# Optimization experiments

Hardware: AMD Instinct MI355X
Metric: run time of the kernel (lower is better)

## Reference

```python
import jax, jax.numpy as jnp
import numpy as np

N, E = 50000, 800000          # nodes, edges
IN, H1, D1 = 128, 8, 32       # gcn1: 8 heads x 32 -> concat 256
HID1 = H1 * D1                # 256
HID2 = 128                    # gcn2: 1 head x 128
FC1, OUT = 512, 1
NEG_SLOPE = 0.2


def _nrm(k, shape, s=0.05):
    return jax.random.normal(k, shape, jnp.float32) * s


def setup_inputs() -> dict:
    key = jax.random.key(0)
    ks = jax.random.split(key, 16)
    return {
        "x": jax.random.normal(ks[0], (N, IN), jnp.float32),
        "edge_index": jax.random.randint(ks[1], (2, E), 0, N, dtype=jnp.int32),
        # gcn1 params
        "W1": _nrm(ks[2], (IN, H1 * D1)),
        "att_src1": _nrm(ks[3], (H1, D1)),
        "att_dst1": _nrm(ks[4], (H1, D1)),
        "b1": jnp.zeros((HID1,), jnp.float32),
        # gcn2 params (1 head)
        "W2": _nrm(ks[5], (HID1, HID2)),
        "att_src2": _nrm(ks[6], (1, HID2)),
        "att_dst2": _nrm(ks[7], (1, HID2)),
        "b2": jnp.zeros((HID2,), jnp.float32),
        # fc head
        "fcW1": _nrm(ks[8], (HID2, FC1)),
        "fcb1": jnp.zeros((FC1,), jnp.float32),
        "fcW2": _nrm(ks[9], (FC1, OUT)),
        "fcb2": jnp.zeros((OUT,), jnp.float32),
    }


def gat_layer(x, src, dst, W, a_src, a_dst, b, heads, dim):
    """PyG GATConv (eval mode): gather -> segment-softmax over dst -> scatter."""
    n = x.shape[0]
    h = (x @ W).reshape(n, heads, dim)                     # [N,H,D]
    a_s = jnp.einsum('nhd,hd->nh', h, a_src)               # [N,H]
    a_d = jnp.einsum('nhd,hd->nh', h, a_dst)
    e = jax.nn.leaky_relu(a_s[src] + a_d[dst], NEG_SLOPE)  # [E,H]
    m = jax.ops.segment_max(e, dst, num_segments=n)        # [N,H]
    m = jnp.where(jnp.isfinite(m), m, 0.0)                 # empty segments
    ex = jnp.exp(e - m[dst])
    denom = jax.ops.segment_sum(ex, dst, num_segments=n)
    alpha = ex / (denom[dst] + 1e-16)                      # [E,H]
    out = jax.ops.segment_sum(h[src] * alpha[:, :, None], dst, num_segments=n)
    return out.reshape(n, heads * dim) + b, alpha


def reference(x, edge_index, W1, att_src1, att_dst1, b1,
              W2, att_src2, att_dst2, b2, fcW1, fcb1, fcW2, fcb2):
    src, dst = edge_index[0], edge_index[1]
    x1, alpha1 = gat_layer(x, src, dst, W1, att_src1, att_dst1, b1, H1, D1)
    x1 = jax.nn.elu(x1)
    x2, alpha2 = gat_layer(x1, src, dst, W2, att_src2, att_dst2, b2, 1, HID2)
    x2 = jax.nn.relu(x2)
    h = jax.nn.relu(x2 @ fcW1 + fcb1)
    out = h @ fcW2 + fcb2                                  # [N,1]
    return out, alpha1, alpha2
```

## Files before the change

kernel.cpp:

```cpp
#include <hip/hip_runtime.h>
#include <hip/hip_bf16.h>
#include <hip/hip_fp8.h>
#include <math.h>

#define NN 50000
#define EE 800000
#define IN_DIM 128
#define H1 8
#define D1 32
#define HID1 256
#define HID2 128
#define FC1 512
#define NEG_SLOPE 0.2f
#define NREP 16

typedef short v8s __attribute__((ext_vector_type(8)));
typedef float v4f __attribute__((ext_vector_type(4)));
typedef float v2f __attribute__((ext_vector_type(2)));
typedef unsigned int v4u __attribute__((ext_vector_type(4)));

__device__ __forceinline__ float bf2f(unsigned short u) {
    unsigned int x = ((unsigned int)u) << 16;
    return __uint_as_float(x);
}
__device__ __forceinline__ unsigned short f2bf(float v) {
    __hip_bfloat16 h = __float2bfloat16(v);
    return *(unsigned short*)&h;
}
__device__ __forceinline__ unsigned char f2f8(float v) {
    __hip_fp8_e4m3 t(v);
    return (unsigned char)t.__x;
}
__device__ __forceinline__ float f8tof(unsigned char u) {
    __hip_fp8_e4m3 t;
    t.__x = (__hip_fp8_storage_t)u;
    return (float)t;
}

__device__ __forceinline__ void f8x4(unsigned int w, float& f0, float& f1, float& f2, float& f3) {
#if __has_builtin(__builtin_amdgcn_cvt_pk_f32_fp8)
    v2f lo = __builtin_amdgcn_cvt_pk_f32_fp8((int)w, false);
    v2f hi = __builtin_amdgcn_cvt_pk_f32_fp8((int)w, true);
    f0 = lo[0]; f1 = lo[1]; f2 = hi[0]; f3 = hi[1];
#else
    f0 = f8tof((unsigned char)(w & 0xff));
    f1 = f8tof((unsigned char)((w >> 8) & 0xff));
    f2 = f8tof((unsigned char)((w >> 16) & 0xff));
    f3 = f8tof((unsigned char)(w >> 24));
#endif
}


__global__ void hist_kernel(const int* __restrict__ dst, int* __restrict__ counts_rep) {
    int e = blockIdx.x * blockDim.x + threadIdx.x;
    if (e >= EE) return;
    int r = blockIdx.x & (NREP - 1);
    atomicAdd(&counts_rep[r * NN + dst[e]], 1);
}

__global__ void reduce_kernel(const int* __restrict__ counts_rep, int* __restrict__ counts_total) {
    int d = blockIdx.x * blockDim.x + threadIdx.x;
    if (d >= NN) return;
    int t = 0;
    #pragma unroll
    for (int r = 0; r < NREP; r++) t += counts_rep[r * NN + d];
    counts_total[d] = t;
}

__global__ __launch_bounds__(256) void scan_a_kernel(const int* __restrict__ counts,
                                                     int* __restrict__ excl,
                                                     int* __restrict__ bsum, int n) {
    __shared__ int wsum[4];
    int tid = threadIdx.x;
    int base = blockIdx.x * 1024 + tid * 4;
    int v0 = 0, v1 = 0, v2 = 0, v3 = 0;
    if (base + 3 < n) {
        int4 t = *(const int4*)(counts + base);
        v0 = t.x; v1 = t.y; v2 = t.z; v3 = t.w;
    } else {
        if (base + 0 < n) v0 = counts[base + 0];
        if (base + 1 < n) v1 = counts[base + 1];
        if (base + 2 < n) v2 = counts[base + 2];
        if (base + 3 < n) v3 = counts[base + 3];
    }
    int tot = v0 + v1 + v2 + v3;
    int lane = tid & 63;
    int w = tid >> 6;
    int x = tot;
    #pragma unroll
    for (int off = 1; off < 64; off <<= 1) {
        int y = __shfl_up(x, off);
        if (lane >= off) x += y;
    }
    if (lane == 63) wsum[w] = x;
    __syncthreads();
    int woff = 0;
    for (int i = 0; i < w; i++) woff += wsum[i];
    int et = woff + x - tot;
    if (base + 0 < n) excl[base + 0] = et;
    if (base + 1 < n) excl[base + 1] = et + v0;
    if (base + 2 < n) excl[base + 2] = et + v0 + v1;
    if (base + 3 < n) excl[base + 3] = et + v0 + v1 + v2;
    if (tid == 255) bsum[blockIdx.x] = woff + x;
}

__global__ __launch_bounds__(64) void scan_b_kernel(int* __restrict__ bsum,
                                                    int* __restrict__ row_ptr, int nb, int n) {
    int lane = threadIdx.x;
    int v = (lane < nb) ? bsum[lane] : 0;
    int x = v;
    #pragma unroll
    for (int off = 1; off < 64; off <<= 1) {
        int y = __shfl_up(x, off);
        if (lane >= off) x += y;
    }
    if (lane < nb) bsum[lane] = x - v;
    if (lane == 63) row_ptr[n] = x;
}

__global__ __launch_bounds__(256) void scan_c_kernel(const int* __restrict__ excl,
                                                     const int* __restrict__ bsum,
                                                     int* __restrict__ row_ptr, int n) {
    int base = blockIdx.x * 1024 + threadIdx.x * 4;
    int off = bsum[blockIdx.x];
    #pragma unroll
    for (int j = 0; j < 4; j++) {
        int i = base + j;
        if (i < n) row_ptr[i] = excl[i] + off;
    }
}

__global__ void base_kernel(const int* __restrict__ row_ptr, const int* __restrict__ counts_rep,
                            int* __restrict__ cursor_rep) {
    int d = blockIdx.x * blockDim.x + threadIdx.x;
    if (d >= NN) return;
    int running = row_ptr[d];
    #pragma unroll
    for (int r = 0; r < NREP; r++) {
        cursor_rep[r * NN + d] = running;
        running += counts_rep[r * NN + d];
    }
}

__global__ void scatter_kernel(const int* __restrict__ src, const int* __restrict__ dst,
                               int* __restrict__ cursor_rep, int2* __restrict__ pairs) {
    int e = blockIdx.x * blockDim.x + threadIdx.x;
    if (e >= EE) return;
    int r = blockIdx.x & (NREP - 1);
    int d = dst[e];
    int p = atomicAdd(&cursor_rep[r * NN + d], 1);
    pairs[p] = make_int2(e, src[e]);
}


__device__ __forceinline__ void pack_one(const float* __restrict__ B,
                                         __hip_bfloat16* __restrict__ Bp,
                                         int K, int N, int idx) {
    int k = idx / N, n = idx % N;
    int ntile = n >> 4, ks = k >> 5, kk = k & 31;
    int lane = (n & 15) | ((kk >> 3) << 4);
    int j = kk & 7;
    int KS = K >> 5;
    Bp[((size_t)(ntile * KS + ks) * 64 + lane) * 8 + j] = __float2bfloat16(B[idx]);
}

__global__ void prep_kernel(const float* __restrict__ x, __hip_bfloat16* __restrict__ xbf,
                            const float* __restrict__ W1, __hip_bfloat16* __restrict__ W1p,
                            const float* __restrict__ W2, __hip_bfloat16* __restrict__ W2p,
                            const float* __restrict__ fcW1, __hip_bfloat16* __restrict__ fW1p) {
    int i = blockIdx.x * blockDim.x + threadIdx.x;
    const int N0 = NN * IN_DIM;
    const int N1 = N0 + IN_DIM * HID1;
    const int N2 = N1 + HID1 * HID2;
    const int N3 = N2 + HID2 * FC1;
    if (i < N0) xbf[i] = __float2bfloat16(x[i]);
    else if (i < N1) pack_one(W1, W1p, IN_DIM, HID1, i - N0);
    else if (i < N2) pack_one(W2, W2p, HID1, HID2, i - N1);
    else if (i < N3) pack_one(fcW1, fW1p, HID2, FC1, i - N2);
}


template <int ATT>
__global__ __launch_bounds__(256) void mgemm_kernel(const __hip_bfloat16* __restrict__ A,
                                                    const __hip_bfloat16* __restrict__ Bp,
                                                    unsigned char* __restrict__ Cf8,
                                                    const float* __restrict__ as_w,
                                                    const float* __restrict__ ad_w,
                                                    float* __restrict__ a_s,
                                                    float* __restrict__ a_d,
                                                    int M, int K, int N) {
    int w = threadIdx.x >> 6, l = threadIdx.x & 63;
    int bm = blockIdx.x * 128 + w * 32;
    int bn = blockIdx.y * 64;
    int lr = l & 15, lk = l >> 4;
    int KS = K >> 5;
    const short* Ab = (const short*)A;
    const short* Bb = (const short*)Bp;
    v4f acc[2][4];
    #pragma unroll
    for (int mi = 0; mi < 2; mi++)
        #pragma unroll
        for (int nt = 0; nt < 4; nt++) acc[mi][nt] = (v4f)(0.f);
    for (int ks = 0; ks < KS; ks++) {
        v8s a[2];
        #pragma unroll
        for (int mi = 0; mi < 2; mi++) {
            int gm = bm + mi * 16 + lr;
            a[mi] = (gm < M) ? *(const v8s*)(Ab + (size_t)gm * K + ks * 32 + lk * 8)
                             : (v8s)(short)0;
        }
        #pragma unroll
        for (int nt = 0; nt < 4; nt++) {
            int ntile = (bn >> 4) + nt;
            v8s b = *(const v8s*)(Bb + ((size_t)(ntile * KS + ks) * 64 + l) * 8);
            acc[0][nt] = __builtin_amdgcn_mfma_f32_16x16x32_bf16(a[0], b, acc[0][nt], 0, 0, 0);
            acc[1][nt] = __builtin_amdgcn_mfma_f32_16x16x32_bf16(a[1], b, acc[1][nt], 0, 0, 0);
        }
    }
    #pragma unroll
    for (int mi = 0; mi < 2; mi++) {
        #pragma unroll
        for (int nt = 0; nt < 4; nt++) {
            int gn = bn + nt * 16 + lr;
            #pragma unroll
            for (int j = 0; j < 4; j++) {
                int gm = bm + mi * 16 + lk * 4 + j;
                if (gm < M)
                    Cf8[(size_t)gm * N + gn] = f2f8(acc[mi][nt][j]);
            }
        }
    }
    float ws0 = as_w[bn + lr], ws1 = as_w[bn + 16 + lr];
    float ws2 = as_w[bn + 32 + lr], ws3 = as_w[bn + 48 + lr];
    float wd0 = ad_w[bn + lr], wd1 = ad_w[bn + 16 + lr];
    float wd2 = ad_w[bn + 32 + lr], wd3 = ad_w[bn + 48 + lr];
    float sA[2][4], dA[2][4], sB[2][4], dB[2][4];
    #pragma unroll
    for (int mi = 0; mi < 2; mi++)
        #pragma unroll
        for (int j = 0; j < 4; j++) {
            if constexpr (ATT == 1) {
                sA[mi][j] = acc[mi][0][j] * ws0 + acc[mi][1][j] * ws1;
                sB[mi][j] = acc[mi][2][j] * ws2 + acc[mi][3][j] * ws3;
                dA[mi][j] = acc[mi][0][j] * wd0 + acc[mi][1][j] * wd1;
                dB[mi][j] = acc[mi][2][j] * wd2 + acc[mi][3][j] * wd3;
            } else {
                sA[mi][j] = acc[mi][0][j] * ws0 + acc[mi][1][j] * ws1
                          + acc[mi][2][j] * ws2 + acc[mi][3][j] * ws3;
                dA[mi][j] = acc[mi][0][j] * wd0 + acc[mi][1][j] * wd1
                          + acc[mi][2][j] * wd2 + acc[mi][3][j] * wd3;
                sB[mi][j] = 0.f; dB[mi][j] = 0.f;
            }
        }
    #pragma unroll
    for (int off = 1; off < 16; off <<= 1) {
        #pragma unroll
        for (int mi = 0; mi < 2; mi++)
            #pragma unroll
            for (int j = 0; j < 4; j++) {
                sA[mi][j] += __shfl_xor(sA[mi][j], off);
                dA[mi][j] += __shfl_xor(dA[mi][j], off);
                if constexpr (ATT == 1) {
                    sB[mi][j] += __shfl_xor(sB[mi][j], off);
                    dB[mi][j] += __shfl_xor(dB[mi][j], off);
                }
            }
    }
    if (lr == 0) {
        #pragma unroll
        for (int mi = 0; mi < 2; mi++)
            #pragma unroll
            for (int j = 0; j < 4; j++) {
                int row = bm + mi * 16 + lk * 4 + j;
                if (row < M) {
                    if constexpr (ATT == 1) {
                        int h0 = bn >> 5;
                        a_s[(size_t)row * 8 + h0]     = sA[mi][j];
                        a_s[(size_t)row * 8 + h0 + 1] = sB[mi][j];
                        a_d[(size_t)row * 8 + h0]     = dA[mi][j];
                        a_d[(size_t)row * 8 + h0 + 1] = dB[mi][j];
                    } else {
                        atomicAdd(&a_s[row], sA[mi][j]);
                        atomicAdd(&a_d[row], dA[mi][j]);
                    }
                }
            }
    }
}


__global__ __launch_bounds__(256) void fc_mfma_kernel(const __hip_bfloat16* __restrict__ A,
                                                      const __hip_bfloat16* __restrict__ Bp,
                                                      const float* __restrict__ fcb1,
                                                      const float* __restrict__ fcW2,
                                                      const float* __restrict__ fcb2,
                                                      float* __restrict__ out) {
    __shared__ float red[4][32];
    int w = threadIdx.x >> 6, l = threadIdx.x & 63;
    int bm = blockIdx.x * 32;
    int lr = l & 15, lk = l >> 4;
    const int K = HID2, KS = K >> 5;
    const short* Ab = (const short*)A;
    const short* Bb = (const short*)Bp;
    v4f acc[2][8];
    #pragma unroll
    for (int mi = 0; mi < 2; mi++)
        #pragma unroll
        for (int nt = 0; nt < 8; nt++) acc[mi][nt] = (v4f)(0.f);
    for (int ks = 0; ks < KS; ks++) {
        v8s a[2];
        #pragma unroll
        for (int mi = 0; mi < 2; mi++) {
            int gm = bm + mi * 16 + lr;
            a[mi] = (gm < NN) ? *(const v8s*)(Ab + (size_t)gm * K + ks * 32 + lk * 8)
                              : (v8s)(short)0;
        }
        #pragma unroll
        for (int nt = 0; nt < 8; nt++) {
            int ntile = w * 8 + nt;
            v8s b = *(const v8s*)(Bb + ((size_t)(ntile * KS + ks) * 64 + l) * 8);
            acc[0][nt] = __builtin_amdgcn_mfma_f32_16x16x32_bf16(a[0], b, acc[0][nt], 0, 0, 0);
            acc[1][nt] = __builtin_amdgcn_mfma_f32_16x16x32_bf16(a[1], b, acc[1][nt], 0, 0, 0);
        }
    }
    float p[2][4];
    #pragma unroll
    for (int mi = 0; mi < 2; mi++)
        #pragma unroll
        for (int j = 0; j < 4; j++) p[mi][j] = 0.f;
    #pragma unroll
    for (int nt = 0; nt < 8; nt++) {
        int col = w * 128 + nt * 16 + lr;
        float b1v = fcb1[col], w2v = fcW2[col];
        #pragma unroll
        for (int mi = 0; mi < 2; mi++) {
            #pragma unroll
            for (int j = 0; j < 4; j++) {
                float v = acc[mi][nt][j] + b1v;
                p[mi][j] += ((v > 0.f) ? v : 0.f) * w2v;
            }
        }
    }
    #pragma unroll
    for (int mi = 0; mi < 2; mi++)
        #pragma unroll
        for (int j = 0; j < 4; j++) {
            float v = p[mi][j];
            v += __shfl_xor(v, 1);
            v += __shfl_xor(v, 2);
            v += __shfl_xor(v, 4);
            v += __shfl_xor(v, 8);
            p[mi][j] = v;
        }
    if (lr == 0) {
        #pragma unroll
        for (int mi = 0; mi < 2; mi++)
            #pragma unroll
            for (int j = 0; j < 4; j++) red[w][mi * 16 + lk * 4 + j] = p[mi][j];
    }
    __syncthreads();
    int tid = threadIdx.x;
    if (tid < 32) {
        int gm = bm + tid;
        if (gm < NN)
            out[gm] = red[0][tid] + red[1][tid] + red[2][tid] + red[3][tid] + fcb2[0];
    }
}


template <int KM>
__device__ __forceinline__ void gat1_fast(int lane, int start, int cnt,
                                          const int2* __restrict__ pairs,
                                          const float* __restrict__ a_s, float ad,
                                          const unsigned char* __restrict__ hf8,
                                          float* __restrict__ alpha1_out,
                                          float& acc0, float& acc1, float& acc2, float& acc3) {
    int h = lane & 7, j = lane >> 3;
    int hl = lane >> 3;
    int cl = min(lane, cnt - 1);
    int2 ep = pairs[start + cl];
    int e_all = ep.x, s_all = ep.y;
    unsigned int loff = (unsigned int)(lane << 2);

    if constexpr (KM <= 4) {
        constexpr int NB = KM * 8;
        int sj[KM];
        float ev[KM];
        #pragma unroll
        for (int k = 0; k < KM; k++) {
            int idx = j + k * 8;
            sj[k] = __shfl(s_all, idx);
            ev[k] = a_s[(size_t)sj[k] * 8 + h];
        }
        unsigned int qt[NB];
        #pragma unroll
        for (int e = 0; e < NB; e++) {
            int sje = __shfl(s_all, e);
            qt[e] = *(const unsigned int*)(hf8 + (((unsigned int)sje << 8) | loff));
        }
        float ex[KM];
        #pragma unroll
        for (int k = 0; k < KM; k++) {
            int idx = j + k * 8;
            float v = ev[k] + ad;
            v = (v >= 0.f) ? v : NEG_SLOPE * v;
            ex[k] = (idx < cnt) ? v : -INFINITY;
        }
        float m = ex[0];
        #pragma unroll
        for (int k = 1; k < KM; k++) m = fmaxf(m, ex[k]);
        m = fmaxf(m, __shfl_xor(m, 8));
        m = fmaxf(m, __shfl_xor(m, 16));
        m = fmaxf(m, __shfl_xor(m, 32));
        float s = 0.f;
        #pragma unroll
        for (int k = 0; k < KM; k++) {
            ex[k] = expf(ex[k] - m);
            s += ex[k];
        }
        s += __shfl_xor(s, 8);
        s += __shfl_xor(s, 16);
        s += __shfl_xor(s, 32);
        float inv = 1.f / (s + 1e-16f);
        #pragma unroll
        for (int k = 0; k < KM; k++) ex[k] *= inv;
        #pragma unroll
        for (int k = 0; k < KM; k++) {
            int idx = j + k * 8;
            int eo = __shfl(e_all, idx);
            if (idx < cnt) alpha1_out[(size_t)eo * 8 + h] = ex[k];
        }
        #pragma unroll
        for (int e = 0; e < NB; e++) {
            float At = __shfl(ex[e >> 3], (e & 7) * 8 + hl);
            float f0, f1, f2, f3;
            f8x4(qt[e], f0, f1, f2, f3);
            acc0 += At * f0;
            acc1 += At * f1;
            acc2 += At * f2;
            acc3 += At * f3;
        }
    } else {
        float ex[KM];
        int sj[KM];
        #pragma unroll
        for (int k = 0; k < KM; k++) {
            int idx = j + k * 8;
            sj[k] = __shfl(s_all, idx);
            float v = a_s[(size_t)sj[k] * 8 + h] + ad;
            v = (v >= 0.f) ? v : NEG_SLOPE * v;
            ex[k] = (idx < cnt) ? v : -INFINITY;
        }
        float m = ex[0];
        #pragma unroll
        for (int k = 1; k < KM; k++) m = fmaxf(m, ex[k]);
        m = fmaxf(m, __shfl_xor(m, 8));
        m = fmaxf(m, __shfl_xor(m, 16));
        m = fmaxf(m, __shfl_xor(m, 32));
        float s = 0.f;
        #pragma unroll
        for (int k = 0; k < KM; k++) {
            ex[k] = expf(ex[k] - m);
            s += ex[k];
        }
        s += __shfl_xor(s, 8);
        s += __shfl_xor(s, 16);
        s += __shfl_xor(s, 32);
        float inv = 1.f / (s + 1e-16f);
        #pragma unroll
        for (int k = 0; k < KM; k++) ex[k] *= inv;
        #pragma unroll
        for (int k = 0; k < KM; k++) {
            int idx = j + k * 8;
            int eo = __shfl(e_all, idx);
            if (idx < cnt) alpha1_out[(size_t)eo * 8 + h] = ex[k];
        }
        unsigned int pk[KM];
        #pragma unroll
        for (int k = 0; k < KM; k++)
            pk[k] = ((unsigned int)sj[k] << 16) | (unsigned int)f2bf(ex[k]);
        int rounds = (cnt + 7) >> 3;
        #pragma unroll
        for (int K = 0; K < KM; K++) {
            if (K < rounds) {
                float At[8];
                unsigned int qt[8];
                #pragma unroll
                for (int t = 0; t < 8; t++) {
                    unsigned int wv = (unsigned int)__shfl((int)pk[K], t * 8 + hl);
                    At[t] = bf2f((unsigned short)wv);
                    qt[t] = *(const unsigned int*)(hf8 + (((wv >> 16) << 8) | loff));
                }
                #pragma unroll
                for (int t = 0; t < 8; t++) {
                    float f0, f1, f2, f3;
                    f8x4(qt[t], f0, f1, f2, f3);
                    acc0 += At[t] * f0;
                    acc1 += At[t] * f1;
                    acc2 += At[t] * f2;
                    acc3 += At[t] * f3;
                }
            }
        }
    }
}

__global__ __launch_bounds__(256) void gat1_kernel(const int* __restrict__ row_ptr,
                                                   const int2* __restrict__ pairs,
                                                   const float* __restrict__ a_s,
                                                   const float* __restrict__ a_d,
                                                   const unsigned char* __restrict__ h1f8,
                                                   const float* __restrict__ b1,
                                                   float* __restrict__ alpha1_out,
                                                   __hip_bfloat16* __restrict__ x1bf) {
    int wv = threadIdx.x >> 6, lane = threadIdx.x & 63;
    int n = blockIdx.x * 4 + wv;
    if (n >= NN) return;
    int start = row_ptr[n], end = row_ptr[n + 1];
    int cnt = end - start;
    int h = lane & 7, j = lane >> 3;
    int hl = lane >> 3;
    unsigned int loff = (unsigned int)(lane << 2);
    float acc0 = 0.f, acc1 = 0.f, acc2 = 0.f, acc3 = 0.f;
    if (cnt > 0 && cnt <= 64) {
        float ad = a_d[(size_t)n * 8 + h];
        if (cnt <= 8)
            gat1_fast<1>(lane, start, cnt, pairs, a_s, ad, h1f8, alpha1_out, acc0, acc1, acc2, acc3);
        else if (cnt <= 16)
            gat1_fast<2>(lane, start, cnt, pairs, a_s, ad, h1f8, alpha1_out, acc0, acc1, acc2, acc3);
        else if (cnt <= 24)
            gat1_fast<3>(lane, start, cnt, pairs, a_s, ad, h1f8, alpha1_out, acc0, acc1, acc2, acc3);
        else if (cnt <= 32)
            gat1_fast<4>(lane, start, cnt, pairs, a_s, ad, h1f8, alpha1_out, acc0, acc1, acc2, acc3);
        else
            gat1_fast<8>(lane, start, cnt, pairs, a_s, ad, h1f8, alpha1_out, acc0, acc1, acc2, acc3);
    } else if (cnt > 64) {
        float ad = a_d[(size_t)n * 8 + h];
        float m = -INFINITY;
        for (int p = start + j; p < end; p += 8) {
            float v = a_s[(size_t)pairs[p].y * 8 + h] + ad;
            v = (v >= 0.f) ? v : NEG_SLOPE * v;
            m = fmaxf(m, v);
        }
        m = fmaxf(m, __shfl_xor(m, 8));
        m = fmaxf(m, __shfl_xor(m, 16));
        m = fmaxf(m, __shfl_xor(m, 32));
        float s = 0.f;
        for (int p = start + j; p < end; p += 8) {
            float v = a_s[(size_t)pairs[p].y * 8 + h] + ad;
            v = (v >= 0.f) ? v : NEG_SLOPE * v;
            s += expf(v - m);
        }
        s += __shfl_xor(s, 8);
        s += __shfl_xor(s, 16);
        s += __shfl_xor(s, 32);
        float inv = 1.f / (s + 1e-16f);
        for (int p = start + j; p < end; p += 8) {
            int2 ep = pairs[p];
            float v = a_s[(size_t)ep.y * 8 + h] + ad;
            v = (v >= 0.f) ? v : NEG_SLOPE * v;
            alpha1_out[(size_t)ep.x * 8 + h] = expf(v - m) * inv;
        }
        float mh = __shfl(m, hl);
        float invh = __shfl(inv, hl);
        float adh = __shfl(ad, hl);
        for (int p = start; p < end; p++) {
            int sp = pairs[p].y;
            float v = a_s[(size_t)sp * 8 + hl] + adh;
            v = (v >= 0.f) ? v : NEG_SLOPE * v;
            float al = expf(v - mh) * invh;
            unsigned int q = *(const unsigned int*)(h1f8 + (((unsigned int)sp << 8) | loff));
            float f0, f1, f2, f3;
            f8x4(q, f0, f1, f2, f3);
            acc0 += al * f0;
            acc1 += al * f1;
            acc2 += al * f2;
            acc3 += al * f3;
        }
    }
    float4 bb = *(const float4*)(b1 + lane * 4);
    float r0 = acc0 + bb.x, r1 = acc1 + bb.y, r2 = acc2 + bb.z, r3 = acc3 + bb.w;
    r0 = (r0 > 0.f) ? r0 : expf(r0) - 1.f;
    r1 = (r1 > 0.f) ? r1 : expf(r1) - 1.f;
    r2 = (r2 > 0.f) ? r2 : expf(r2) - 1.f;
    r3 = (r3 > 0.f) ? r3 : expf(r3) - 1.f;
    ushort4 o;
    o.x = f2bf(r0); o.y = f2bf(r1); o.z = f2bf(r2); o.w = f2bf(r3);
    *(ushort4*)((unsigned short*)x1bf + (size_t)n * HID1 + lane * 4) = o;
}


template <int RM>
__device__ __forceinline__ void gat2_fast(int lane, int start, int cnt, int r, int c,
                                          const int2* __restrict__ pairs,
                                          const float* __restrict__ a_s, float ad,
                                          const unsigned char* __restrict__ hf8,
                                          float* __restrict__ alpha2_out,
                                          float& acc0, float& acc1, float& acc2, float& acc3) {
    bool act = lane < cnt;
    int ii = min(lane, cnt - 1);
    int2 ep = pairs[start + ii];
    int sj = ep.y;
    float asv = a_s[sj];
    unsigned int coff = (unsigned int)(c << 2);
    constexpr int NB = RM * 4;
    unsigned int qt[NB];
    #pragma unroll
    for (int t = 0; t < NB; t++) {
        int je = (t >> 2) * 8 + (t & 3) * 2 + r;
        int sje = __shfl(sj, je);
        qt[t] = *(const unsigned int*)(hf8 + (((unsigned int)sje << 7) | coff));
    }
    float v = asv + ad;
    v = (v >= 0.f) ? v : NEG_SLOPE * v;
    float e = act ? v : -INFINITY;
    float m = e;
    #pragma unroll
    for (int off = 1; off < 64; off <<= 1) m = fmaxf(m, __shfl_xor(m, off));
    float ex = expf(e - m);
    float s = ex;
    #pragma unroll
    for (int off = 1; off < 64; off <<= 1) s += __shfl_xor(s, off);
    float al = ex / (s + 1e-16f);
    if (act) alpha2_out[ep.x] = al;
    #pragma unroll
    for (int t = 0; t < NB; t++) {
        int je = (t >> 2) * 8 + (t & 3) * 2 + r;
        float At = __shfl(al, je);
        float f0, f1, f2, f3;
        f8x4(qt[t], f0, f1, f2, f3);
        acc0 += At * f0;
        acc1 += At * f1;
        acc2 += At * f2;
        acc3 += At * f3;
    }
}

__global__ __launch_bounds__(256) void gat2_kernel(const int* __restrict__ row_ptr,
                                                   const int2* __restrict__ pairs,
                                                   const float* __restrict__ a_s,
                                                   const float* __restrict__ a_d,
                                                   const unsigned char* __restrict__ h2f8,
                                                   const float* __restrict__ b2,
                                                   float* __restrict__ alpha2_out,
                                                   __hip_bfloat16* __restrict__ x2bf) {
    int wv = threadIdx.x >> 6, lane = threadIdx.x & 63;
    int n = blockIdx.x * 4 + wv;
    if (n >= NN) return;
    int start = row_ptr[n], end = row_ptr[n + 1];
    int cnt = end - start;
    int r = lane >> 5, c = lane & 31;
    float acc0 = 0.f, acc1 = 0.f, acc2 = 0.f, acc3 = 0.f;
    if (cnt > 0 && cnt <= 64) {
        float ad = a_d[n];
        if (cnt <= 8)
            gat2_fast<1>(lane, start, cnt, r, c, pairs, a_s, ad, h2f8, alpha2_out, acc0, acc1, acc2, acc3);
        else if (cnt <= 16)
            gat2_fast<2>(lane, start, cnt, r, c, pairs, a_s, ad, h2f8, alpha2_out, acc0, acc1, acc2, acc3);
        else if (cnt <= 32)
            gat2_fast<4>(lane, start, cnt, r, c, pairs, a_s, ad, h2f8, alpha2_out, acc0, acc1, acc2, acc3);
        else
            gat2_fast<8>(lane, start, cnt, r, c, pairs, a_s, ad, h2f8, alpha2_out, acc0, acc1, acc2, acc3);
    } else if (cnt > 64) {
        float ad = a_d[n];
        unsigned int coff = (unsigned int)(c << 2);
        float m = -INFINITY;
        for (int p = start + lane; p < end; p += 64) {
            float v = a_s[pairs[p].y] + ad;
            v = (v >= 0.f) ? v : NEG_SLOPE * v;
            m = fmaxf(m, v);
        }
        for (int off = 32; off; off >>= 1) m = fmaxf(m, __shfl_xor(m, off));
        float s = 0.f;
        for (int p = start + lane; p < end; p += 64) {
            float v = a_s[pairs[p].y] + ad;
            v = (v >= 0.f) ? v : NEG_SLOPE * v;
            s += expf(v - m);
        }
        for (int off = 32; off; off >>= 1) s += __shfl_xor(s, off);
        float inv = 1.f / (s + 1e-16f);
        for (int p = start + lane; p < end; p += 64) {
            int2 ep = pairs[p];
            float v = a_s[ep.y] + ad;
            v = (v >= 0.f) ? v : NEG_SLOPE * v;
            alpha2_out[ep.x] = expf(v - m) * inv;
        }
        for (int p = start + r; p < end; p += 2) {
            int sp = pairs[p].y;
            float v = a_s[sp] + ad;
            v = (v >= 0.f) ? v : NEG_SLOPE * v;
            float al = expf(v - m) * inv;
            unsigned int q = *(const unsigned int*)(h2f8 + (((unsigned int)sp << 7) | coff));
            float f0, f1, f2, f3;
            f8x4(q, f0, f1, f2, f3);
            acc0 += al * f0;
            acc1 += al * f1;
            acc2 += al * f2;
            acc3 += al * f3;
        }
    }
    acc0 += __shfl_xor(acc0, 32);
    acc1 += __shfl_xor(acc1, 32);
    acc2 += __shfl_xor(acc2, 32);
    acc3 += __shfl_xor(acc3, 32);
    if (r == 0) {
        float4 bb = *(const float4*)(b2 + c * 4);
        float r0 = acc0 + bb.x, r1 = acc1 + bb.y, r2 = acc2 + bb.z, r3 = acc3 + bb.w;
        r0 = (r0 > 0.f) ? r0 : 0.f;
        r1 = (r1 > 0.f) ? r1 : 0.f;
        r2 = (r2 > 0.f) ? r2 : 0.f;
        r3 = (r3 > 0.f) ? r3 : 0.f;
        ushort4 o;
        o.x = f2bf(r0); o.y = f2bf(r1); o.z = f2bf(r2); o.w = f2bf(r3);
        *(ushort4*)((unsigned short*)x2bf + (size_t)n * HID2 + c * 4) = o;
    }
}


extern "C" void kernel_launch(void* const* d_in, const int* in_sizes, int n_in,
                              void* d_out, int out_size, void* d_ws, size_t ws_size,
                              hipStream_t stream) {
    (void)in_sizes; (void)n_in; (void)out_size; (void)ws_size;
    const float* x        = (const float*)d_in[0];
    const int*   eindex   = (const int*)d_in[1];
    const float* W1       = (const float*)d_in[2];
    const float* att_src1 = (const float*)d_in[3];
    const float* att_dst1 = (const float*)d_in[4];
    const float* b1       = (const float*)d_in[5];
    const float* W2       = (const float*)d_in[6];
    const float* att_src2 = (const float*)d_in[7];
    const float* att_dst2 = (const float*)d_in[8];
    const float* b2       = (const float*)d_in[9];
    const float* fcW1     = (const float*)d_in[10];
    const float* fcb1     = (const float*)d_in[11];
    const float* fcW2     = (const float*)d_in[12];
    const float* fcb2     = (const float*)d_in[13];

    const int* src = eindex;
    const int* dst = eindex + EE;

    float* out_n      = (float*)d_out;
    float* alpha1_out = out_n + NN;
    float* alpha2_out = alpha1_out + (size_t)EE * 8;

    char* ws = (char*)d_ws;
    size_t off = 0;
    auto alloc = [&](size_t bytes) {
        size_t o = off;
        off = (off + bytes + 255) & ~(size_t)255;
        return o;
    };
    size_t o_rowptr = alloc((NN + 1) * sizeof(int));
    size_t o_crep   = alloc((size_t)NREP * NN * sizeof(int));
    size_t o_curs   = alloc((size_t)NREP * NN * sizeof(int));
    size_t o_ctot   = alloc(NN * sizeof(int));
    size_t o_excl   = alloc(NN * sizeof(int));
    size_t o_bsum   = alloc(64 * sizeof(int));
    size_t o_pairs  = alloc((size_t)EE * sizeof(int2));
    size_t o_as1    = alloc((size_t)NN * H1 * sizeof(float));
    size_t o_ad1    = alloc((size_t)NN * H1 * sizeof(float));
    size_t o_as2    = alloc((size_t)NN * sizeof(float));
    size_t o_ad2    = alloc((size_t)NN * sizeof(float));
    size_t o_h1f8   = alloc((size_t)NN * HID1);
    size_t o_xbf    = alloc((size_t)NN * IN_DIM * sizeof(__hip_bfloat16));
    size_t o_x1bf   = alloc((size_t)NN * HID1 * sizeof(__hip_bfloat16));
    size_t o_h2f8   = alloc((size_t)NN * HID2);
    size_t o_x2bf   = alloc((size_t)NN * HID2 * sizeof(__hip_bfloat16));
    size_t o_W1p    = alloc((size_t)IN_DIM * HID1 * sizeof(__hip_bfloat16));
    size_t o_W2p    = alloc((size_t)HID1 * HID2 * sizeof(__hip_bfloat16));
    size_t o_fW1p   = alloc((size_t)HID2 * FC1 * sizeof(__hip_bfloat16));

    int*   row_ptr    = (int*)(ws + o_rowptr);
    int*   counts_rep = (int*)(ws + o_crep);
    int*   cursor_rep = (int*)(ws + o_curs);
    int*   counts_tot = (int*)(ws + o_ctot);
    int*   excl       = (int*)(ws + o_excl);
    int*   bsum       = (int*)(ws + o_bsum);
    int2*  pairs      = (int2*)(ws + o_pairs);
    float* a_s1       = (float*)(ws + o_as1);
    float* a_d1       = (float*)(ws + o_ad1);
    float* a_s2       = (float*)(ws + o_as2);
    float* a_d2       = (float*)(ws + o_ad2);
    unsigned char*  h1f8  = (unsigned char*)(ws + o_h1f8);
    __hip_bfloat16* xbf   = (__hip_bfloat16*)(ws + o_xbf);
    __hip_bfloat16* x1bf  = (__hip_bfloat16*)(ws + o_x1bf);
    unsigned char*  h2f8  = (unsigned char*)(ws + o_h2f8);
    __hip_bfloat16* x2bf  = (__hip_bfloat16*)(ws + o_x2bf);
    __hip_bfloat16* W1p   = (__hip_bfloat16*)(ws + o_W1p);
    __hip_bfloat16* W2p   = (__hip_bfloat16*)(ws + o_W2p);
    __hip_bfloat16* fW1p  = (__hip_bfloat16*)(ws + o_fW1p);

    const int SCAN_NB = (NN + 1023) / 1024;
    const int PREP_N = NN * IN_DIM + IN_DIM * HID1 + HID1 * HID2 + HID2 * FC1;

    hipMemsetAsync(counts_rep, 0, (size_t)NREP * NN * sizeof(int), stream);
    hipMemsetAsync(a_s2, 0, NN * sizeof(float), stream);
    hipMemsetAsync(a_d2, 0, NN * sizeof(float), stream);

    hist_kernel<<<(EE + 255) / 256, 256, 0, stream>>>(dst, counts_rep);
    reduce_kernel<<<(NN + 255) / 256, 256, 0, stream>>>(counts_rep, counts_tot);
    scan_a_kernel<<<SCAN_NB, 256, 0, stream>>>(counts_tot, excl, bsum, NN);
    scan_b_kernel<<<1, 64, 0, stream>>>(bsum, row_ptr, SCAN_NB, NN);
    scan_c_kernel<<<SCAN_NB, 256, 0, stream>>>(excl, bsum, row_ptr, NN);
    base_kernel<<<(NN + 255) / 256, 256, 0, stream>>>(row_ptr, counts_rep, cursor_rep);
    scatter_kernel<<<(EE + 255) / 256, 256, 0, stream>>>(src, dst, cursor_rep, pairs);

    prep_kernel<<<(PREP_N + 255) / 256, 256, 0, stream>>>(x, xbf, W1, W1p, W2, W2p, fcW1, fW1p);

    mgemm_kernel<1><<<dim3((NN + 127) / 128, HID1 / 64), 256, 0, stream>>>(
        xbf, W1p, h1f8, att_src1, att_dst1, a_s1, a_d1, NN, IN_DIM, HID1);
    gat1_kernel<<<(NN + 3) / 4, 256, 0, stream>>>(row_ptr, pairs, a_s1, a_d1,
                                                  h1f8, b1, alpha1_out, x1bf);

    mgemm_kernel<2><<<dim3((NN + 127) / 128, HID2 / 64), 256, 0, stream>>>(
        x1bf, W2p, h2f8, att_src2, att_dst2, a_s2, a_d2, NN, HID1, HID2);
    gat2_kernel<<<(NN + 3) / 4, 256, 0, stream>>>(row_ptr, pairs, a_s2, a_d2,
                                                  h2f8, b2, alpha2_out, x2bf);

    fc_mfma_kernel<<<(NN + 31) / 32, 256, 0, stream>>>(x2bf, fW1p, fcb1, fcW2, fcb2, out_n);
}
```

Measured before the change: 259.6 us.

## Build CSR with range-partitioned shared-memory histogram and scatter

Replaces the replicated global-atomic histogram, reduce, base and scatter kernels with two kernels. In each, a block owns a 1024-node range, scans the whole dst array and does LDS atomics only for edges landing in its range. This removes global atomic contention and the 16x replicated count buffers plus their memset and reduction. The cost is that all 49 blocks read every edge (about 49x redundant reads of dst/src), and with only 49 blocks most of the GPU sits idle. Within-segment edge order is also nondeterministic.

```diff
diff --git a/kernel.cpp b/kernel.cpp
--- a/kernel.cpp
+++ b/kernel.cpp
@@ -12,7 +12,7 @@
 #define HID2 128
 #define FC1 512
 #define NEG_SLOPE 0.2f
-#define NREP 16
+#define RANGE 1024
 
 typedef short v8s __attribute__((ext_vector_type(8)));
 typedef float v4f __attribute__((ext_vector_type(4)));
@@ -51,20 +51,27 @@
 }
 
 
-__global__ void hist_kernel(const int* __restrict__ dst, int* __restrict__ counts_rep) {
-    int e = blockIdx.x * blockDim.x + threadIdx.x;
-    if (e >= EE) return;
-    int r = blockIdx.x & (NREP - 1);
-    atomicAdd(&counts_rep[r * NN + dst[e]], 1);
-}
-
-__global__ void reduce_kernel(const int* __restrict__ counts_rep, int* __restrict__ counts_total) {
-    int d = blockIdx.x * blockDim.x + threadIdx.x;
-    if (d >= NN) return;
-    int t = 0;
-    #pragma unroll
-    for (int r = 0; r < NREP; r++) t += counts_rep[r * NN + d];
-    counts_total[d] = t;
+__global__ __launch_bounds__(1024) void hist_ranged_kernel(const int* __restrict__ dst,
+                                                           int* __restrict__ counts) {
+    __shared__ int hcnt[RANGE];
+    int tid = threadIdx.x;
+    int base = blockIdx.x * RANGE;
+    hcnt[tid] = 0;
+    __syncthreads();
+    for (int e0 = tid * 4; e0 < EE; e0 += 1024 * 4) {
+        int4 d4 = *(const int4*)(dst + e0);
+        unsigned int a = (unsigned int)(d4.x - base);
+        unsigned int b = (unsigned int)(d4.y - base);
+        unsigned int c = (unsigned int)(d4.z - base);
+        unsigned int d = (unsigned int)(d4.w - base);
+        if (a < RANGE) atomicAdd(&hcnt[a], 1);
+        if (b < RANGE) atomicAdd(&hcnt[b], 1);
+        if (c < RANGE) atomicAdd(&hcnt[c], 1);
+        if (d < RANGE) atomicAdd(&hcnt[d], 1);
+    }
+    __syncthreads();
+    int g = base + tid;
+    if (g < NN) counts[g] = hcnt[tid];
 }
 
 __global__ __launch_bounds__(256) void scan_a_kernel(const int* __restrict__ counts,
@@ -130,26 +137,28 @@
     }
 }
 
-__global__ void base_kernel(const int* __restrict__ row_ptr, const int* __restrict__ counts_rep,
-                            int* __restrict__ cursor_rep) {
-    int d = blockIdx.x * blockDim.x + threadIdx.x;
-    if (d >= NN) return;
-    int running = row_ptr[d];
-    #pragma unroll
-    for (int r = 0; r < NREP; r++) {
-        cursor_rep[r * NN + d] = running;
-        running += counts_rep[r * NN + d];
-    }
-}
-
-__global__ void scatter_kernel(const int* __restrict__ src, const int* __restrict__ dst,
-                               int* __restrict__ cursor_rep, int2* __restrict__ pairs) {
-    int e = blockIdx.x * blockDim.x + threadIdx.x;
-    if (e >= EE) return;
-    int r = blockIdx.x & (NREP - 1);
-    int d = dst[e];
-    int p = atomicAdd(&cursor_rep[r * NN + d], 1);
-    pairs[p] = make_int2(e, src[e]);
+__global__ __launch_bounds__(1024) void scatter_ranged_kernel(const int* __restrict__ src,
+                                                              const int* __restrict__ dst,
+                                                              const int* __restrict__ row_ptr,
+                                                              int2* __restrict__ pairs) {
+    __shared__ int cur[RANGE];
+    int tid = threadIdx.x;
+    int base = blockIdx.x * RANGE;
+    int g = base + tid;
+    cur[tid] = (g < NN) ? row_ptr[g] : 0;
+    __syncthreads();
+    for (int e0 = tid * 4; e0 < EE; e0 += 1024 * 4) {
+        int4 d4 = *(const int4*)(dst + e0);
+        int4 s4 = *(const int4*)(src + e0);
+        unsigned int a = (unsigned int)(d4.x - base);
+        unsigned int b = (unsigned int)(d4.y - base);
+        unsigned int c = (unsigned int)(d4.z - base);
+        unsigned int d = (unsigned int)(d4.w - base);
+        if (a < RANGE) { int p = atomicAdd(&cur[a], 1); pairs[p] = make_int2(e0 + 0, s4.x); }
+        if (b < RANGE) { int p = atomicAdd(&cur[b], 1); pairs[p] = make_int2(e0 + 1, s4.y); }
+        if (c < RANGE) { int p = atomicAdd(&cur[c], 1); pairs[p] = make_int2(e0 + 2, s4.z); }
+        if (d < RANGE) { int p = atomicAdd(&cur[d], 1); pairs[p] = make_int2(e0 + 3, s4.w); }
+    }
 }
 
 
@@ -751,8 +760,6 @@
         return o;
     };
     size_t o_rowptr = alloc((NN + 1) * sizeof(int));
-    size_t o_crep   = alloc((size_t)NREP * NN * sizeof(int));
-    size_t o_curs   = alloc((size_t)NREP * NN * sizeof(int));
     size_t o_ctot   = alloc(NN * sizeof(int));
     size_t o_excl   = alloc(NN * sizeof(int));
     size_t o_bsum   = alloc(64 * sizeof(int));
@@ -771,8 +778,6 @@
     size_t o_fW1p   = alloc((size_t)HID2 * FC1 * sizeof(__hip_bfloat16));
 
     int*   row_ptr    = (int*)(ws + o_rowptr);
-    int*   counts_rep = (int*)(ws + o_crep);
-    int*   cursor_rep = (int*)(ws + o_curs);
     int*   counts_tot = (int*)(ws + o_ctot);
     int*   excl       = (int*)(ws + o_excl);
     int*   bsum       = (int*)(ws + o_bsum);
@@ -791,19 +796,17 @@
     __hip_bfloat16* fW1p  = (__hip_bfloat16*)(ws + o_fW1p);
 
     const int SCAN_NB = (NN + 1023) / 1024;
+    const int NRANGE = (NN + RANGE - 1) / RANGE;
     const int PREP_N = NN * IN_DIM + IN_DIM * HID1 + HID1 * HID2 + HID2 * FC1;
 
-    hipMemsetAsync(counts_rep, 0, (size_t)NREP * NN * sizeof(int), stream);
     hipMemsetAsync(a_s2, 0, NN * sizeof(float), stream);
     hipMemsetAsync(a_d2, 0, NN * sizeof(float), stream);
 
-    hist_kernel<<<(EE + 255) / 256, 256, 0, stream>>>(dst, counts_rep);
-    reduce_kernel<<<(NN + 255) / 256, 256, 0, stream>>>(counts_rep, counts_tot);
+    hist_ranged_kernel<<<NRANGE, 1024, 0, stream>>>(dst, counts_tot);
     scan_a_kernel<<<SCAN_NB, 256, 0, stream>>>(counts_tot, excl, bsum, NN);
     scan_b_kernel<<<1, 64, 0, stream>>>(bsum, row_ptr, SCAN_NB, NN);
     scan_c_kernel<<<SCAN_NB, 256, 0, stream>>>(excl, bsum, row_ptr, NN);
-    base_kernel<<<(NN + 255) / 256, 256, 0, stream>>>(row_ptr, counts_rep, cursor_rep);
-    scatter_kernel<<<(EE + 255) / 256, 256, 0, stream>>>(src, dst, cursor_rep, pairs);
+    scatter_ranged_kernel<<<NRANGE, 1024, 0, stream>>>(src, dst, row_ptr, pairs);
 
     prep_kernel<<<(PREP_N + 255) / 256, 256, 0, stream>>>(x, xbf, W1, W1p, W2, W2p, fcW1, fW1p);
 
```

Measured after the change: 410.3 us. 1.58x slower.
